# Performance work log

Measured on AMD Instinct MI355X. Metric: run time of the kernel, lower is better.

## Reference

```python
import jax, jax.numpy as jnp
import numpy as np
import math


def _align_seq_len(e, target_n):
    # e: (B, H, N_enc, hd) -> (B, H, target_n, hd) via bilinear resize on sqrt grid
    B, H, N_enc, D = e.shape
    if N_enc == target_n:
        return e
    h_e = int(math.sqrt(N_enc))
    h_t = int(math.sqrt(target_n))
    img = jnp.transpose(e, (0, 1, 3, 2)).reshape(B, H, D, h_e, h_e)
    img = jax.image.resize(img, (B, H, D, h_t, h_t), method='bilinear')
    return jnp.transpose(img.reshape(B, H, D, target_n), (0, 1, 3, 2))


def setup_inputs() -> dict:
    key = jax.random.key(0)
    ks = jax.random.split(key, 7)
    B, N, D, H = 4, 1024, 1152, 16
    hd = D // H
    N_enc = 1024
    s_in = 1.0 / math.sqrt(D)
    return {
        'x': jax.random.normal(ks[0], (B, N, D), jnp.float32),
        'enc_k': jax.random.normal(ks[1], (B, H, N_enc, hd), jnp.float32),
        'enc_v': jax.random.normal(ks[2], (B, H, N_enc, hd), jnp.float32),
        'qkv_w': jax.random.normal(ks[3], (3 * D, D), jnp.float32) * s_in,
        'qkv_b': jax.random.normal(ks[4], (3 * D,), jnp.float32) * 0.02,
        'proj_w': jax.random.normal(ks[5], (D, D), jnp.float32) * s_in,
        'proj_b': jax.random.normal(ks[6], (D,), jnp.float32) * 0.02,
        'stage': 2,
    }


def reference(x, enc_k, enc_v, qkv_w, qkv_b, proj_w, proj_b, stage):
    B, N, C = x.shape
    H = enc_k.shape[1]
    hd = C // H
    scale = hd ** (-0.5)

    qkv = (x @ qkv_w.T + qkv_b).reshape(B, N, 3, H, hd)
    qkv = jnp.transpose(qkv, (2, 0, 3, 1, 4))  # (3, B, H, N, hd)
    q, k, v = qkv[0], qkv[1], qkv[2]

    distill_loss = jnp.float32(0.0)
    if stage == 1:
        ek = _align_seq_len(enc_k, N)
        ev = _align_seq_len(enc_v, N)
        attn = jax.nn.softmax(jnp.einsum('bhnd,bhmd->bhnm', q * scale, ek), axis=-1)
        x_out = jnp.einsum('bhnm,bhmd->bhnd', attn, ev)
    elif stage == 2:
        ek = _align_seq_len(enc_k, N)
        ev = _align_seq_len(enc_v, N)
        attn_own = jax.nn.softmax(jnp.einsum('bhnd,bhmd->bhnm', q * scale, k), axis=-1)
        x_out = jnp.einsum('bhnm,bhmd->bhnd', attn_own, v)
        qd = jax.lax.stop_gradient(q)
        attn_enc = jax.nn.softmax(jnp.einsum('bhnd,bhmd->bhnm', qd * scale, ek), axis=-1)
        o_star = jax.lax.stop_gradient(jnp.einsum('bhnm,bhmd->bhnd', attn_enc, ev))
        distill_loss = jnp.mean((x_out - o_star) ** 2)
    else:
        attn = jax.nn.softmax(jnp.einsum('bhnd,bhmd->bhnm', q * scale, k), axis=-1)
        x_out = jnp.einsum('bhnm,bhmd->bhnd', attn, v)

    x_out = jnp.transpose(x_out, (0, 2, 1, 3)).reshape(B, N, C)
    out = x_out @ proj_w.T + proj_b
    return out, distill_loss
```

## Files before the change

kernel.cpp:

```cpp
#include <hip/hip_runtime.h>
#include <hip/hip_bf16.h>

#define PB 4
#define PN 1024
#define PC 1152
#define PH 16
#define PHD 72
#define BH 64
#define QKV_COLS 3456
#define OUT_ELEMS ((size_t)PB*PN*PC)
#define K_DIM 1152

#define CHUNK_HALVES 6144
#define HEAD_HALVES (16*CHUNK_HALVES)
#define BUF_HALVES ((size_t)BH*HEAD_HALVES)

typedef _Float16 half8_t __attribute__((ext_vector_type(8)));
typedef _Float16 half4_t __attribute__((ext_vector_type(4)));
typedef float float4v __attribute__((ext_vector_type(4)));

#define QSCALE (0.11785113019775792f * 1.4426950408889634f)

__device__ __forceinline__ void load16_lds(const _Float16* g, _Float16* l) {
    __builtin_amdgcn_global_load_lds(
        (const __attribute__((address_space(1))) void*)g,
        (__attribute__((address_space(3))) void*)l, 16, 0, 0);
}

__global__ __launch_bounds__(256) void f32_to_f16(
    const float* __restrict__ in, _Float16* __restrict__ out, int n8)
{
    int i = blockIdx.x * 256 + threadIdx.x;
    if (i >= n8) return;
    float4 a = ((const float4*)in)[2 * i];
    float4 b = ((const float4*)in)[2 * i + 1];
    half8_t h;
    h[0] = (_Float16)a.x; h[1] = (_Float16)a.y; h[2] = (_Float16)a.z; h[3] = (_Float16)a.w;
    h[4] = (_Float16)b.x; h[5] = (_Float16)b.y; h[6] = (_Float16)b.z; h[7] = (_Float16)b.w;
    ((half8_t*)out)[i] = h;
}

__global__ __launch_bounds__(256) void zero_qpad(_Float16* __restrict__ qh)
{
    int i = blockIdx.x * 256 + threadIdx.x;
    int chunk = i / 192, within = i - chunk * 192;
    half8_t z = {};
    *(half8_t*)(qh + (size_t)chunk * CHUNK_HALVES + 4608 + within * 8) = z;
}

__global__ __launch_bounds__(256) void enc_convert(
    const float* __restrict__ ek, const float* __restrict__ ev,
    _Float16* __restrict__ ekh, _Float16* __restrict__ evth)
{
    const int bh = blockIdx.y, nblk = blockIdx.x, t = threadIdx.x;
    const float* ksrc = ek + ((size_t)bh * PN + nblk * 64) * PHD;
    const float* vsrc = ev + ((size_t)bh * PN + nblk * 64) * PHD;
    _Float16* kdst = ekh  + ((size_t)bh * 16 + nblk) * CHUNK_HALVES;
    _Float16* vdst = evth + ((size_t)bh * 16 + nblk) * CHUNK_HALVES;
    for (int i = t; i < 64 * 18; i += 256) {
        int n = i / 18, d4 = (i % 18) * 4;
        float4 kv = *(const float4*)&ksrc[n * PHD + d4];
        float4 vv = *(const float4*)&vsrc[n * PHD + d4];
        float ka[4] = {kv.x, kv.y, kv.z, kv.w};
        float va[4] = {vv.x, vv.y, vv.z, vv.w};
#pragma unroll
        for (int kk = 0; kk < 4; ++kk) {
            int d = d4 + kk;
            kdst[(d >> 3) * 512 + n * 8 + (d & 7)] = (_Float16)ka[kk];
            vdst[(n >> 3) * 768 + d * 8 + (n & 7)] = (_Float16)va[kk];
        }
    }
}

template<int MODE>
__global__ __launch_bounds__(256) void gemm_mfma(
    const _Float16* __restrict__ A, const _Float16* __restrict__ Bm,
    const float* __restrict__ bias,
    _Float16* __restrict__ qh, _Float16* __restrict__ kh,
    _Float16* __restrict__ vth, float* __restrict__ out, int c_tiles)
{
    const int t    = threadIdx.x;
    const int lane = t & 63;
    const int w    = t >> 6;
    const int wm   = w >> 1, wn = w & 1;
    const int lrow = lane & 15, quad = lane >> 4;

    const int per_group = c_tiles * 8;
    const int g  = blockIdx.x / per_group;
    const int r_ = blockIdx.x - g * per_group;
    const int m0 = (g * 8 + (r_ & 7)) * 128;
    const int c0 = (r_ >> 3) * 128;

    const bool tr = (MODE == 1) || (c0 < 2 * PC);

    __shared__ _Float16 As[8192];
    __shared__ _Float16 Bs[8192];

    int rowS[4], koff[4], ldsOff[4];
#pragma unroll
    for (int i = 0; i < 4; ++i) {
        int idx = w * 256 + i * 64 + lane;
        int kt2 = idx >> 9, qq = (idx >> 7) & 3;
        rowS[i]   = idx & 127;
        koff[i]   = kt2 * 32 + qq * 8;
        ldsOff[i] = idx * 8;
    }

    const _Float16* aBase = A  + (size_t)m0 * K_DIM;
    const _Float16* bBase = Bm + (size_t)c0 * K_DIM;

    float4v acc[4][4];
#pragma unroll
    for (int ti = 0; ti < 4; ++ti)
#pragma unroll
        for (int tj = 0; tj < 4; ++tj)
            acc[ti][tj] = (float4v){0.f, 0.f, 0.f, 0.f};

    for (int kb = 0; kb < K_DIM; kb += 64) {
        __syncthreads();
#pragma unroll
        for (int i = 0; i < 4; ++i) {
            load16_lds(aBase + (size_t)rowS[i] * K_DIM + kb + koff[i], &As[ldsOff[i]]);
            load16_lds(bBase + (size_t)rowS[i] * K_DIM + kb + koff[i], &Bs[ldsOff[i]]);
        }
        __syncthreads();
#pragma unroll
        for (int s = 0; s < 2; ++s) {
            half8_t af[4], bf[4];
#pragma unroll
            for (int ti = 0; ti < 4; ++ti)
                af[ti] = *(const half8_t*)&As[(((s * 4 + quad) * 128) + wm * 64 + ti * 16 + lrow) * 8];
#pragma unroll
            for (int tj = 0; tj < 4; ++tj)
                bf[tj] = *(const half8_t*)&Bs[(((s * 4 + quad) * 128) + wn * 64 + tj * 16 + lrow) * 8];
            if (tr) {
#pragma unroll
                for (int ti = 0; ti < 4; ++ti)
#pragma unroll
                    for (int tj = 0; tj < 4; ++tj)
                        acc[ti][tj] = __builtin_amdgcn_mfma_f32_16x16x32_f16(
                            bf[tj], af[ti], acc[ti][tj], 0, 0, 0);
            } else {
#pragma unroll
                for (int ti = 0; ti < 4; ++ti)
#pragma unroll
                    for (int tj = 0; tj < 4; ++tj)
                        acc[ti][tj] = __builtin_amdgcn_mfma_f32_16x16x32_f16(
                            af[ti], bf[tj], acc[ti][tj], 0, 0, 0);
            }
        }
    }

    if (MODE == 1) {
#pragma unroll
        for (int tj = 0; tj < 4; ++tj) {
            int cg = c0 + wn * 64 + tj * 16 + quad * 4;
            float4v bv = *(const float4v*)&bias[cg];
#pragma unroll
            for (int ti = 0; ti < 4; ++ti) {
                int m = m0 + wm * 64 + ti * 16 + lrow;
                float4v o;
#pragma unroll
                for (int r = 0; r < 4; ++r) o[r] = acc[ti][tj][r] + bv[r];
                *(float4v*)&out[(size_t)m * PC + cg] = o;
            }
        }
    } else if (tr) {
        const int jq = c0 / PC;
        const float mulv = (jq == 0) ? QSCALE : 1.f;
        _Float16* dstp = (jq == 0) ? qh : kh;
#pragma unroll
        for (int tj = 0; tj < 4; ++tj) {
            int cg  = c0 + wn * 64 + tj * 16 + quad * 4;
            int rem = cg - jq * PC;
            int h   = rem / PHD;
            int ds  = rem - h * PHD;
            float4v bv = *(const float4v*)&bias[cg];
#pragma unroll
            for (int ti = 0; ti < 4; ++ti) {
                int m = m0 + wm * 64 + ti * 16 + lrow;
                int b = m >> 10, n = m & 1023;
                size_t chunk = ((size_t)(b * PH + h) * 16 + (n >> 6)) * CHUNK_HALVES;
                half4_t hv;
#pragma unroll
                for (int r = 0; r < 4; ++r)
                    hv[r] = (_Float16)((acc[ti][tj][r] + bv[r]) * mulv);
                *(half4_t*)&dstp[chunk + (ds >> 3) * 512 + (n & 63) * 8 + (ds & 7)] = hv;
            }
        }
    } else {
#pragma unroll
        for (int tj = 0; tj < 4; ++tj) {
            int c   = c0 + wn * 64 + tj * 16 + lrow;
            int rem = c - 2 * PC;
            int h   = rem / PHD;
            int d   = rem - h * PHD;
            float bv = bias[c];
#pragma unroll
            for (int ti = 0; ti < 4; ++ti) {
                int mg = m0 + wm * 64 + ti * 16 + quad * 4;
                int b = mg >> 10, n = mg & 1023;
                size_t chunk = ((size_t)(b * PH + h) * 16 + (n >> 6)) * CHUNK_HALVES;
                half4_t hv;
#pragma unroll
                for (int r = 0; r < 4; ++r)
                    hv[r] = (_Float16)(acc[ti][tj][r] + bv);
                *(half4_t*)&vth[chunk + ((n & 63) >> 3) * 768 + d * 8 + (n & 7)] = hv;
            }
        }
    }
}

__device__ __forceinline__ void attn_step(
    const half8_t* qf, const _Float16* Ks, const _Float16* Vts, _Float16* Pw,
    float4v* O, float& m_run, float& l_run, int ln, int quad)
{
    float4v accS[4];
#pragma unroll
    for (int ct = 0; ct < 4; ++ct) accS[ct] = (float4v){0.f, 0.f, 0.f, 0.f};
#pragma unroll
    for (int ks = 0; ks < 3; ++ks) {
#pragma unroll
        for (int ct = 0; ct < 4; ++ct) {
            half8_t kf = *(const half8_t*)&Ks[(((ks * 4 + quad) * 64) + ct * 16 + ln) * 8];
            accS[ct] = __builtin_amdgcn_mfma_f32_16x16x32_f16(kf, qf[ks], accS[ct], 0, 0, 0);
        }
    }

    float mx = -1e30f;
#pragma unroll
    for (int ct = 0; ct < 4; ++ct)
#pragma unroll
        for (int r = 0; r < 4; ++r) mx = fmaxf(mx, accS[ct][r]);
    mx = fmaxf(mx, __shfl_xor(mx, 16));
    mx = fmaxf(mx, __shfl_xor(mx, 32));
    float m_new = fmaxf(m_run, mx);
    float alpha = exp2f(m_run - m_new);
    m_run = m_new;

    float lsum = 0.f;
    const int pbase = (quad >> 1) * 128 + ln * 8 + (quad & 1) * 4;
#pragma unroll
    for (int ct = 0; ct < 4; ++ct) {
        half4_t pk;
#pragma unroll
        for (int r = 0; r < 4; ++r) {
            float p = exp2f(accS[ct][r] - m_new);
            lsum += p;
            pk[r] = (_Float16)p;
        }
        *(half4_t*)&Pw[pbase + ct * 256] = pk;
    }
    lsum += __shfl_xor(lsum, 16);
    lsum += __shfl_xor(lsum, 32);
    l_run = l_run * alpha + lsum;

#pragma unroll
    for (int ct = 0; ct < 5; ++ct) O[ct] *= alpha;

#pragma unroll
    for (int ks = 0; ks < 2; ++ks) {
        half8_t pf = *(const half8_t*)&Pw[(ks * 4 + quad) * 128 + ln * 8];
#pragma unroll
        for (int ct = 0; ct < 5; ++ct) {
            half8_t vf = *(const half8_t*)&Vts[(((ks * 4 + quad) * 96) + ct * 16 + ln) * 8];
            O[ct] = __builtin_amdgcn_mfma_f32_16x16x32_f16(vf, pf, O[ct], 0, 0, 0);
        }
    }
}

__global__ __launch_bounds__(256, 4) void attn_fused(
    const _Float16* __restrict__ qh, const _Float16* __restrict__ kh,
    const _Float16* __restrict__ vth,
    const _Float16* __restrict__ ekh, const _Float16* __restrict__ evth,
    _Float16* __restrict__ xouth, float* __restrict__ loss_out)
{
    const int t = threadIdx.x;
    const int lane = t & 63;
    const int w = t >> 6;
    const int ln = lane & 15;
    const int quad = lane >> 4;

    const int lid  = blockIdx.x;
    const int bh   = (lid & 7) * 8 + ((lid >> 3) >> 4);
    const int nblk = (lid >> 3) & 15;

    __shared__ _Float16 Ks[CHUNK_HALVES];
    __shared__ _Float16 Vs[CHUNK_HALVES];
    __shared__ _Float16 Ps[4096];
    __shared__ float red[256];

    _Float16* Pw = Ps + w * 1024;

    const _Float16* qc = qh + ((size_t)bh * 16 + nblk) * CHUNK_HALVES;
    half8_t qf[3];
#pragma unroll
    for (int ks = 0; ks < 3; ++ks)
        qf[ks] = *(const half8_t*)&qc[(((ks * 4 + quad) * 64) + w * 16 + ln) * 8];

    const _Float16* kbo = kh   + (size_t)bh * HEAD_HALVES;
    const _Float16* vbo = vth  + (size_t)bh * HEAD_HALVES;
    const _Float16* kbe = ekh  + (size_t)bh * HEAD_HALVES;
    const _Float16* vbe = evth + (size_t)bh * HEAD_HALVES;

    float4v Oo[5], Oe[5];
#pragma unroll
    for (int ct = 0; ct < 5; ++ct) {
        Oo[ct] = (float4v){0.f, 0.f, 0.f, 0.f};
        Oe[ct] = (float4v){0.f, 0.f, 0.f, 0.f};
    }
    float m_o = -1e30f, l_o = 0.f;
    float m_e = -1e30f, l_e = 0.f;

    for (int kt = 0; kt < 16; ++kt) {
        const _Float16* kc = kbo + (size_t)kt * CHUNK_HALVES;
        const _Float16* vc = vbo + (size_t)kt * CHUNK_HALVES;
        __syncthreads();
#pragma unroll
        for (int i = 0; i < 3; ++i) {
            int u = i * 256 + t;
            load16_lds(kc + u * 8, &Ks[u * 8]);
            load16_lds(vc + u * 8, &Vs[u * 8]);
        }
        __syncthreads();
        attn_step(qf, Ks, Vs, Pw, Oo, m_o, l_o, ln, quad);
    }
    for (int kt = 0; kt < 16; ++kt) {
        const _Float16* kc = kbe + (size_t)kt * CHUNK_HALVES;
        const _Float16* vc = vbe + (size_t)kt * CHUNK_HALVES;
        __syncthreads();
#pragma unroll
        for (int i = 0; i < 3; ++i) {
            int u = i * 256 + t;
            load16_lds(kc + u * 8, &Ks[u * 8]);
            load16_lds(vc + u * 8, &Vs[u * 8]);
        }
        __syncthreads();
        attn_step(qf, Ks, Vs, Pw, Oe, m_e, l_e, ln, quad);
    }

    const float inv_o = 1.0f / l_o;
    const float inv_e = 1.0f / l_e;

    const int b = bh >> 4, h = bh & 15;
    const int nrow = nblk * 64 + w * 16 + ln;

    float lacc = 0.f;
    const size_t rowbase = (size_t)(b * PN + nrow) * PC + h * PHD;
#pragma unroll
    for (int ct = 0; ct < 5; ++ct) {
        int d0 = ct * 16 + quad * 4;
        if (d0 < PHD) {
            half4_t oh;
#pragma unroll
            for (int r = 0; r < 4; ++r) {
                float own = Oo[ct][r] * inv_o;
                oh[r] = (_Float16)own;
                float df = own - Oe[ct][r] * inv_e;
                lacc += df * df;
            }
            *(half4_t*)&xouth[rowbase + d0] = oh;
        }
    }

    red[t] = lacc;
    __syncthreads();
    for (int off = 128; off > 0; off >>= 1) {
        if (t < off) red[t] += red[t + off];
        __syncthreads();
    }
    if (t == 0) atomicAdd(loss_out, red[0] * (1.0f / (float)OUT_ELEMS));
}

extern "C" void kernel_launch(void* const* d_in, const int* in_sizes, int n_in,
                              void* d_out, int out_size, void* d_ws, size_t ws_size,
                              hipStream_t stream)
{
    const float* x      = (const float*)d_in[0];
    const float* enc_k  = (const float*)d_in[1];
    const float* enc_v  = (const float*)d_in[2];
    const float* qkv_w  = (const float*)d_in[3];
    const float* qkv_b  = (const float*)d_in[4];
    const float* proj_w = (const float*)d_in[5];
    const float* proj_b = (const float*)d_in[6];

    float* out = (float*)d_out;

    _Float16* x_h     = (_Float16*)d_ws;
    _Float16* qkvw_h  = x_h + OUT_ELEMS;
    _Float16* projw_h = qkvw_h + (size_t)QKV_COLS * PC;
    _Float16* xout_h  = projw_h + (size_t)PC * PC;
    _Float16* q_h     = xout_h + OUT_ELEMS;
    _Float16* k_h     = q_h  + BUF_HALVES;
    _Float16* vt_h    = k_h  + BUF_HALVES;
    _Float16* ek_h    = vt_h + BUF_HALVES;
    _Float16* evt_h   = ek_h + BUF_HALVES;

    const int n8_x  = (int)(OUT_ELEMS / 8);
    const int n8_qw = QKV_COLS * PC / 8;
    const int n8_pw = PC * PC / 8;

    hipMemsetAsync(out + OUT_ELEMS, 0, sizeof(float), stream);
    zero_qpad<<<768, 256, 0, stream>>>(q_h);

    f32_to_f16<<<(n8_x  + 255) / 256, 256, 0, stream>>>(x,      x_h,     n8_x);
    f32_to_f16<<<(n8_qw + 255) / 256, 256, 0, stream>>>(qkv_w,  qkvw_h,  n8_qw);
    f32_to_f16<<<(n8_pw + 255) / 256, 256, 0, stream>>>(proj_w, projw_h, n8_pw);
    enc_convert<<<dim3(16, BH), 256, 0, stream>>>(enc_k, enc_v, ek_h, evt_h);

    gemm_mfma<0><<<(QKV_COLS / 128) * ((PB * PN) / 128), 256, 0, stream>>>(
        x_h, qkvw_h, qkv_b, q_h, k_h, vt_h, nullptr, QKV_COLS / 128);

    attn_fused<<<16 * BH, 256, 0, stream>>>(
        q_h, k_h, vt_h, ek_h, evt_h, xout_h, out + OUT_ELEMS);

    gemm_mfma<1><<<(PC / 128) * ((PB * PN) / 128), 256, 0, stream>>>(
        xout_h, projw_h, proj_b, nullptr, nullptr, nullptr, out, PC / 128);
}
```

Baseline: 346.8 us.

## Prefetch K/V via registers, lazy softmax rescale, row-sum via ones column in V

Replaces direct global-to-LDS loads with register staging that prefetches the next K/V tile while the current tile is computed, and merges the own and encoder loops into one 32-step loop. The online softmax now rescales only when the running max grows by more than a threshold, which skips most alpha multiplies. The running row sum is dropped and recovered instead from a padding column of V that a new kernel fills with ones, so the PV MFMA produces the denominator. This costs extra registers for the staging buffers and relies on fp16 P values staying in range under the lazy-max rule.

```diff
diff --git a/kernel.cpp b/kernel.cpp
--- a/kernel.cpp
+++ b/kernel.cpp
@@ -46,6 +46,19 @@
     int chunk = i / 192, within = i - chunk * 192;
     half8_t z = {};
     *(half8_t*)(qh + (size_t)chunk * CHUNK_HALVES + 4608 + within * 8) = z;
+}
+
+__global__ __launch_bounds__(256) void ones_vrow(
+    _Float16* __restrict__ vt, _Float16* __restrict__ evt)
+{
+    int i = blockIdx.x * 256 + threadIdx.x;
+    _Float16* base = (i < 8192) ? vt : evt;
+    int j = i & 8191;
+    int chunk = j >> 3, kq = j & 7;
+    half8_t o;
+#pragma unroll
+    for (int r = 0; r < 8; ++r) o[r] = (_Float16)1.0f;
+    *(half8_t*)&base[(size_t)chunk * CHUNK_HALVES + kq * 768 + 576] = o;
 }
 
 __global__ __launch_bounds__(256) void enc_convert(
@@ -213,7 +226,7 @@
 
 __device__ __forceinline__ void attn_step(
     const half8_t* qf, const _Float16* Ks, const _Float16* Vts, _Float16* Pw,
-    float4v* O, float& m_run, float& l_run, int ln, int quad)
+    float4v* O, float& m_run, int ln, int quad)
 {
     float4v accS[4];
 #pragma unroll
@@ -227,36 +240,31 @@
         }
     }
 
-    float mx = -1e30f;
-#pragma unroll
-    for (int ct = 0; ct < 4; ++ct)
-#pragma unroll
-        for (int r = 0; r < 4; ++r) mx = fmaxf(mx, accS[ct][r]);
+    float c0 = fmaxf(fmaxf(accS[0][0], accS[0][1]), fmaxf(accS[0][2], accS[0][3]));
+    float c1 = fmaxf(fmaxf(accS[1][0], accS[1][1]), fmaxf(accS[1][2], accS[1][3]));
+    float c2 = fmaxf(fmaxf(accS[2][0], accS[2][1]), fmaxf(accS[2][2], accS[2][3]));
+    float c3 = fmaxf(fmaxf(accS[3][0], accS[3][1]), fmaxf(accS[3][2], accS[3][3]));
+    float mx = fmaxf(fmaxf(c0, c1), fmaxf(c2, c3));
     mx = fmaxf(mx, __shfl_xor(mx, 16));
     mx = fmaxf(mx, __shfl_xor(mx, 32));
-    float m_new = fmaxf(m_run, mx);
-    float alpha = exp2f(m_run - m_new);
-    m_run = m_new;
-
-    float lsum = 0.f;
+
+    if (__any(mx > m_run + 8.f)) {
+        float m_new = fmaxf(m_run, mx);
+        float alpha = exp2f(m_run - m_new);
+        m_run = m_new;
+#pragma unroll
+        for (int ct = 0; ct < 5; ++ct) O[ct] *= alpha;
+    }
+
     const int pbase = (quad >> 1) * 128 + ln * 8 + (quad & 1) * 4;
 #pragma unroll
     for (int ct = 0; ct < 4; ++ct) {
         half4_t pk;
 #pragma unroll
-        for (int r = 0; r < 4; ++r) {
-            float p = exp2f(accS[ct][r] - m_new);
-            lsum += p;
-            pk[r] = (_Float16)p;
-        }
+        for (int r = 0; r < 4; ++r)
+            pk[r] = (_Float16)exp2f(accS[ct][r] - m_run);
         *(half4_t*)&Pw[pbase + ct * 256] = pk;
     }
-    lsum += __shfl_xor(lsum, 16);
-    lsum += __shfl_xor(lsum, 32);
-    l_run = l_run * alpha + lsum;
-
-#pragma unroll
-    for (int ct = 0; ct < 5; ++ct) O[ct] *= alpha;
 
 #pragma unroll
     for (int ks = 0; ks < 2; ++ks) {
@@ -309,36 +317,45 @@
         Oo[ct] = (float4v){0.f, 0.f, 0.f, 0.f};
         Oe[ct] = (float4v){0.f, 0.f, 0.f, 0.f};
     }
-    float m_o = -1e30f, l_o = 0.f;
-    float m_e = -1e30f, l_e = 0.f;
-
-    for (int kt = 0; kt < 16; ++kt) {
-        const _Float16* kc = kbo + (size_t)kt * CHUNK_HALVES;
-        const _Float16* vc = vbo + (size_t)kt * CHUNK_HALVES;
+    float m_o = -1e30f, m_e = -1e30f;
+
+    half8_t stg[6];
+#pragma unroll
+    for (int i = 0; i < 3; ++i) {
+        int u = i * 256 + t;
+        stg[i]     = *(const half8_t*)(kbo + (size_t)u * 8);
+        stg[i + 3] = *(const half8_t*)(vbo + (size_t)u * 8);
+    }
+
+    for (int s = 0; s < 32; ++s) {
         __syncthreads();
 #pragma unroll
         for (int i = 0; i < 3; ++i) {
             int u = i * 256 + t;
-            load16_lds(kc + u * 8, &Ks[u * 8]);
-            load16_lds(vc + u * 8, &Vs[u * 8]);
+            *(half8_t*)&Ks[u * 8] = stg[i];
+            *(half8_t*)&Vs[u * 8] = stg[i + 3];
         }
         __syncthreads();
-        attn_step(qf, Ks, Vs, Pw, Oo, m_o, l_o, ln, quad);
-    }
-    for (int kt = 0; kt < 16; ++kt) {
-        const _Float16* kc = kbe + (size_t)kt * CHUNK_HALVES;
-        const _Float16* vc = vbe + (size_t)kt * CHUNK_HALVES;
-        __syncthreads();
-#pragma unroll
-        for (int i = 0; i < 3; ++i) {
-            int u = i * 256 + t;
-            load16_lds(kc + u * 8, &Ks[u * 8]);
-            load16_lds(vc + u * 8, &Vs[u * 8]);
-        }
-        __syncthreads();
-        attn_step(qf, Ks, Vs, Pw, Oe, m_e, l_e, ln, quad);
-    }
-
+
+        if (s < 31) {
+            int s1 = s + 1;
+            const _Float16* kc = ((s1 < 16) ? kbo : kbe) + (size_t)(s1 & 15) * CHUNK_HALVES;
+            const _Float16* vc = ((s1 < 16) ? vbo : vbe) + (size_t)(s1 & 15) * CHUNK_HALVES;
+#pragma unroll
+            for (int i = 0; i < 3; ++i) {
+                int u = i * 256 + t;
+                stg[i]     = *(const half8_t*)(kc + (size_t)u * 8);
+                stg[i + 3] = *(const half8_t*)(vc + (size_t)u * 8);
+            }
+            __builtin_amdgcn_sched_barrier(0);
+        }
+
+        if (s < 16) attn_step(qf, Ks, Vs, Pw, Oo, m_o, ln, quad);
+        else        attn_step(qf, Ks, Vs, Pw, Oe, m_e, ln, quad);
+    }
+
+    float l_o = __shfl(Oo[4][0], 32 + ln);
+    float l_e = __shfl(Oe[4][0], 32 + ln);
     const float inv_o = 1.0f / l_o;
     const float inv_e = 1.0f / l_e;
 
@@ -402,6 +419,7 @@
 
     hipMemsetAsync(out + OUT_ELEMS, 0, sizeof(float), stream);
     zero_qpad<<<768, 256, 0, stream>>>(q_h);
+    ones_vrow<<<64, 256, 0, stream>>>(vt_h, evt_h);
 
     f32_to_f16<<<(n8_x  + 255) / 256, 256, 0, stream>>>(x,      x_h,     n8_x);
     f32_to_f16<<<(n8_qw + 255) / 256, 256, 0, stream>>>(qkv_w,  qkvw_h,  n8_qw);
```

After: 670.5 us. 93.3% more time.
